# Optimization experiments

Measured on AMD Instinct MI355X. Metric: run time of the kernel, lower is better.

Reference implementation:

```python
import jax, jax.numpy as jnp
import numpy as np

EMBED_DIM = 1024
N_HEADS = 16
HEAD_DIM = EMBED_DIM // N_HEADS


def setup_inputs() -> dict:
    key = jax.random.key(0)
    k_x, k_wi, k_bi, k_wo, k_bo = jax.random.split(key, 5)
    B, N, C = 4, 2048, EMBED_DIM
    scale = 1.0 / np.sqrt(C)
    return {
        "x": jax.random.normal(k_x, (B, N, C), dtype=jnp.float32),
        "w_in": jax.random.normal(k_wi, (C, 3 * C), dtype=jnp.float32) * scale,
        "b_in": jax.random.normal(k_bi, (3 * C,), dtype=jnp.float32) * 0.01,
        "w_out": jax.random.normal(k_wo, (C, C), dtype=jnp.float32) * scale,
        "b_out": jax.random.normal(k_bo, (C,), dtype=jnp.float32) * 0.01,
    }


def reference(x, w_in, b_in, w_out, b_out):
    B, N, C = x.shape
    H, D = N_HEADS, HEAD_DIM
    qkv = x @ w_in + b_in  # (B, N, 3C)
    q, k, v = jnp.split(qkv, 3, axis=-1)
    # (B, H, N, D)
    q = q.reshape(B, N, H, D).transpose(0, 2, 1, 3)
    k = k.reshape(B, N, H, D).transpose(0, 2, 1, 3)
    v = v.reshape(B, N, H, D).transpose(0, 2, 1, 3)
    # Naive attention: full (B,H,N,N) scores, NO sqrt(d) scaling (as in source)
    scores = jnp.einsum("bhnd,bhmd->bhnm", q, k)
    attn = jax.nn.softmax(scores, axis=-1)
    out = jnp.einsum("bhnm,bhmd->bhnd", attn, v)
    out = out.transpose(0, 2, 1, 3).reshape(B, N, C)
    return out @ w_out + b_out
```

## Files before the change

kernel.cpp:

```cpp
#include <hip/hip_runtime.h>
#include <stdint.h>

typedef __attribute__((ext_vector_type(8))) __bf16 bf8v;
typedef __attribute__((ext_vector_type(4))) float f4v;

__device__ __forceinline__ unsigned short f2bf(float f) {
  union { float f; unsigned u; } v; v.f = f;
  unsigned r = v.u + 0x7fffu + ((v.u >> 16) & 1u);
  return (unsigned short)(r >> 16);
}

__device__ __forceinline__ unsigned pk2bf(float f0, float f1) {
  union { float f; unsigned u; } a, b; a.f = f0; b.f = f1;
  unsigned r0 = a.u + 0x7fffu + ((a.u >> 16) & 1u);
  unsigned r1 = b.u + 0x7fffu + ((b.u >> 16) & 1u);
  return __builtin_amdgcn_perm(r1, r0, 0x07060302u);
}

__device__ __forceinline__ void gl_lds16(const void* g, void* l) {
  __builtin_amdgcn_global_load_lds(
      (__attribute__((address_space(1))) void*)(g),
      (__attribute__((address_space(3))) void*)(l), 16, 0, 0);
}

__global__ void cast_bf16_kernel(const float* __restrict__ in,
                                 unsigned short* __restrict__ out) {
  int i = blockIdx.x * 256 + threadIdx.x;
  float4 v = ((const float4*)in)[i];
  ushort4 o;
  o.x = f2bf(v.x); o.y = f2bf(v.y); o.z = f2bf(v.z); o.w = f2bf(v.w);
  ((ushort4*)out)[i] = o;
}

__global__ void transpose_cast_kernel(const float* __restrict__ in,
                                      unsigned short* __restrict__ out,
                                      int R, int C) {
  __shared__ float tile[32][33];
  int c0 = blockIdx.x * 32, r0 = blockIdx.y * 32;
  int tx = threadIdx.x, ty = threadIdx.y;
#pragma unroll
  for (int j = 0; j < 4; ++j)
    tile[ty + 8 * j][tx] = in[(size_t)(r0 + ty + 8 * j) * C + c0 + tx];
  __syncthreads();
#pragma unroll
  for (int j = 0; j < 4; ++j)
    out[(size_t)(c0 + ty + 8 * j) * R + r0 + tx] = f2bf(tile[tx][ty + 8 * j]);
}

__global__ void transpose_v_kernel(const unsigned short* __restrict__ qkv,
                                   unsigned short* __restrict__ vtg) {
  __shared__ unsigned short tile[32][33];
  int bh = blockIdx.z;
  int d0 = blockIdx.y * 32;
  int n0 = blockIdx.x * 32;
  int b = bh >> 4, h = bh & 15;
  int tx = threadIdx.x, ty = threadIdx.y;
  const unsigned short* src = qkv + (size_t)b * 2048 * 3072 + 2048 + h * 64 + d0;
#pragma unroll
  for (int j = 0; j < 4; ++j)
    tile[ty + 8 * j][tx] = src[(size_t)(n0 + ty + 8 * j) * 3072 + tx];
  __syncthreads();
  unsigned short* dst = vtg + ((size_t)bh * 64) * 2048;
#pragma unroll
  for (int j = 0; j < 4; ++j)
    dst[(size_t)(d0 + ty + 8 * j) * 2048 + n0 + tx] = tile[tx][ty + 8 * j];
}

template <bool OUT_BF16>
__global__ __launch_bounds__(256, 2) void gemm_bt(
    const unsigned short* __restrict__ A,
    const unsigned short* __restrict__ BT,
    const float* __restrict__ bias,
    void* __restrict__ Cp,
    int M, int N, int K) {
  __shared__ __align__(16) unsigned short As[128 * 32];
  __shared__ __align__(16) unsigned short Bs[128 * 32];
  const int tid = threadIdx.x;
  const int wave = tid >> 6, lane = tid & 63;
  const int lo = lane & 15, hi = lane >> 4;
  const int m0 = blockIdx.y * 128, n0 = blockIdx.x * 128;
  const int wm = (wave >> 1) * 64, wn = (wave & 1) * 64;

  f4v acc[4][4] = {};

  const int srow = lane >> 2;
  const int scol = (lane & 3) * 8;

  for (int k0 = 0; k0 < K; k0 += 32) {
#pragma unroll
    for (int p = 0; p < 2; ++p) {
      int r = p * 64 + wave * 16 + srow;
      gl_lds16(A + (size_t)(m0 + r) * K + k0 + scol,
               &As[(p * 64 + wave * 16) * 32]);
      gl_lds16(BT + (size_t)(n0 + r) * K + k0 + scol,
               &Bs[(p * 64 + wave * 16) * 32]);
    }
    __syncthreads();
    bf8v a[4], b[4];
#pragma unroll
    for (int i = 0; i < 4; ++i)
      a[i] = *(const bf8v*)&As[(wm + i * 16 + lo) * 32 + hi * 8];
#pragma unroll
    for (int j = 0; j < 4; ++j)
      b[j] = *(const bf8v*)&Bs[(wn + j * 16 + lo) * 32 + hi * 8];
#pragma unroll
    for (int i = 0; i < 4; ++i)
#pragma unroll
      for (int j = 0; j < 4; ++j)
        acc[i][j] = __builtin_amdgcn_mfma_f32_16x16x32_bf16(a[i], b[j], acc[i][j], 0, 0, 0);
    __syncthreads();
  }

#pragma unroll
  for (int i = 0; i < 4; ++i) {
#pragma unroll
    for (int r = 0; r < 4; ++r) {
      int row = m0 + wm + i * 16 + hi * 4 + r;
#pragma unroll
      for (int j = 0; j < 4; ++j) {
        int col = n0 + wn + j * 16 + lo;
        float v = acc[i][j][r] + bias[col];
        if (OUT_BF16)
          ((unsigned short*)Cp)[(size_t)row * N + col] = f2bf(v);
        else
          ((float*)Cp)[(size_t)row * N + col] = v;
      }
    }
  }
}

#define FSTR 72

__global__ __launch_bounds__(256, 4) void flash_attn(
    const unsigned short* __restrict__ qkv,
    const unsigned short* __restrict__ vtg,
    unsigned short* __restrict__ y) {
  __shared__ __align__(16) unsigned short Ps[128 * FSTR];
  __shared__ __align__(16) unsigned short Kt[64 * FSTR];
  __shared__ __align__(16) unsigned short Vt[64 * FSTR];
  const int tid = threadIdx.x;
  const int wave = tid >> 6, lane = tid & 63;
  const int lo = lane & 15, hi = lane >> 4;
  const int b = blockIdx.z, h = blockIdx.y, q0 = blockIdx.x * 128;
  const size_t base = (size_t)b * 2048 * 3072;
  const int qoff = h * 64, koff = 1024 + h * 64;
  const unsigned short* vsrc = vtg + (size_t)(b * 16 + h) * 64 * 2048;

#pragma unroll
  for (int i = 0; i < 4; ++i) {
    int cid = i * 256 + tid;
    int m = cid >> 3, c = cid & 7;
    *(float4*)&Ps[m * FSTR + c * 8] =
        *(const float4*)(qkv + base + (size_t)(q0 + m) * 3072 + qoff + c * 8);
  }
  __syncthreads();
  bf8v bq[2][2];
#pragma unroll
  for (int qt = 0; qt < 2; ++qt)
#pragma unroll
    for (int ks = 0; ks < 2; ++ks)
      bq[qt][ks] = *(const bf8v*)&Ps[(wave * 32 + qt * 16 + lo) * FSTR + ks * 32 + hi * 8];
  __syncthreads();

  f4v O[2][4] = {};
  float l_st[2] = {0.f, 0.f};

  for (int kt = 0; kt < 32; ++kt) {
    const int mb = kt * 64;
#pragma unroll
    for (int i = 0; i < 2; ++i) {
      int cid = i * 256 + tid;
      int m = cid >> 3, c = cid & 7;
      *(float4*)&Kt[m * FSTR + c * 8] =
          *(const float4*)(qkv + base + (size_t)(mb + m) * 3072 + koff + c * 8);
      *(float4*)&Vt[m * FSTR + c * 8] =
          *(const float4*)(vsrc + (size_t)m * 2048 + mb + c * 8);
    }
    __syncthreads();

    f4v s2[4][2] = {};
#pragma unroll
    for (int ks = 0; ks < 2; ++ks) {
#pragma unroll
      for (int ct = 0; ct < 4; ++ct) {
        bf8v ak = *(const bf8v*)&Kt[(ct * 16 + lo) * FSTR + ks * 32 + hi * 8];
        s2[ct][0] = __builtin_amdgcn_mfma_f32_16x16x32_bf16(ak, bq[0][ks], s2[ct][0], 0, 0, 0);
        s2[ct][1] = __builtin_amdgcn_mfma_f32_16x16x32_bf16(ak, bq[1][ks], s2[ct][1], 0, 0, 0);
      }
    }

#pragma unroll
    for (int qt = 0; qt < 2; ++qt) {
      int prow = (wave * 32 + qt * 16 + lo) * FSTR;
#pragma unroll
      for (int ct = 0; ct < 4; ++ct) {
        float p0 = __expf(s2[ct][qt][0]);
        float p1 = __expf(s2[ct][qt][1]);
        float p2 = __expf(s2[ct][qt][2]);
        float p3 = __expf(s2[ct][qt][3]);
        l_st[qt] += (p0 + p1) + (p2 + p3);
        uint2 w;
        w.x = pk2bf(p0, p1);
        w.y = pk2bf(p2, p3);
        *(uint2*)&Ps[prow + ct * 16 + hi * 4] = w;
      }
    }

#pragma unroll
    for (int ks = 0; ks < 2; ++ks) {
      bf8v ap0 = *(const bf8v*)&Ps[(wave * 32 + lo) * FSTR + ks * 32 + hi * 8];
      bf8v ap1 = *(const bf8v*)&Ps[(wave * 32 + 16 + lo) * FSTR + ks * 32 + hi * 8];
#pragma unroll
      for (int dt = 0; dt < 4; ++dt) {
        bf8v bv = *(const bf8v*)&Vt[(dt * 16 + lo) * FSTR + ks * 32 + hi * 8];
        O[0][dt] = __builtin_amdgcn_mfma_f32_16x16x32_bf16(ap0, bv, O[0][dt], 0, 0, 0);
        O[1][dt] = __builtin_amdgcn_mfma_f32_16x16x32_bf16(ap1, bv, O[1][dt], 0, 0, 0);
      }
    }
    __syncthreads();
  }

#pragma unroll
  for (int qt = 0; qt < 2; ++qt) {
    float lt = l_st[qt];
    lt += __shfl_xor(lt, 16);
    lt += __shfl_xor(lt, 32);
    l_st[qt] = lt;
  }
#pragma unroll
  for (int qt = 0; qt < 2; ++qt) {
#pragma unroll
    for (int r = 0; r < 4; ++r) {
      float lr = __shfl(l_st[qt], hi * 4 + r);
      float inv = 1.f / lr;
      int row = q0 + wave * 32 + qt * 16 + hi * 4 + r;
      size_t orow = ((size_t)b * 2048 + row) * 1024 + h * 64;
#pragma unroll
      for (int dt = 0; dt < 4; ++dt)
        y[orow + dt * 16 + lo] = f2bf(O[qt][dt][r] * inv);
    }
  }
}

extern "C" void kernel_launch(void* const* d_in, const int* in_sizes, int n_in,
                              void* d_out, int out_size, void* d_ws, size_t ws_size,
                              hipStream_t stream) {
  (void)in_sizes; (void)n_in; (void)out_size; (void)ws_size;
  const float* x     = (const float*)d_in[0];
  const float* w_in  = (const float*)d_in[1];
  const float* b_in  = (const float*)d_in[2];
  const float* w_out = (const float*)d_in[3];
  const float* b_out = (const float*)d_in[4];

  unsigned short* xb  = (unsigned short*)d_ws;
  unsigned short* wiT = xb  + (size_t)8192 * 1024;
  unsigned short* woT = wiT + (size_t)3072 * 1024;
  unsigned short* qkv = woT + (size_t)1024 * 1024;
  unsigned short* yb  = qkv + (size_t)8192 * 3072;
  unsigned short* vtg = xb;

  cast_bf16_kernel<<<8192, 256, 0, stream>>>(x, xb);
  transpose_cast_kernel<<<dim3(96, 32), dim3(32, 8), 0, stream>>>(w_in, wiT, 1024, 3072);
  transpose_cast_kernel<<<dim3(32, 32), dim3(32, 8), 0, stream>>>(w_out, woT, 1024, 1024);

  gemm_bt<true><<<dim3(24, 64), 256, 0, stream>>>(xb, wiT, b_in, qkv, 8192, 3072, 1024);
  transpose_v_kernel<<<dim3(64, 2, 64), dim3(32, 8), 0, stream>>>(qkv, vtg);
  flash_attn<<<dim3(16, 16, 4), 256, 0, stream>>>(qkv, vtg, yb);
  gemm_bt<false><<<dim3(8, 64), 256, 0, stream>>>(yb, woT, b_out, d_out, 8192, 1024, 1024);
}
```

Before: 316.7 us.

## Fold log2e into Q projection, use hw exp2, merge weight transposes, smaller out-proj tiles

Pre-scales the Q columns of the QKV projection by log2(e) so the attention softmax can use the hardware exp2 instruction instead of __expf. Merges the two weight transpose-cast launches into one kernel. Adds a 64x128-tile output-projection GEMM to double the block count for the smaller N=1024 GEMM, and switches bf16 packing to the HIP intrinsic. Rounding Q after scaling slightly changes numerics.

```diff
diff --git a/kernel.cpp b/kernel.cpp
--- a/kernel.cpp
+++ b/kernel.cpp
@@ -1,8 +1,11 @@
 #include <hip/hip_runtime.h>
+#include <hip/hip_bf16.h>
 #include <stdint.h>
 
 typedef __attribute__((ext_vector_type(8))) __bf16 bf8v;
 typedef __attribute__((ext_vector_type(4))) float f4v;
+
+#define L2E 1.44269504088896f
 
 __device__ __forceinline__ unsigned short f2bf(float f) {
   union { float f; unsigned u; } v; v.f = f;
@@ -11,10 +14,13 @@
 }
 
 __device__ __forceinline__ unsigned pk2bf(float f0, float f1) {
-  union { float f; unsigned u; } a, b; a.f = f0; b.f = f1;
-  unsigned r0 = a.u + 0x7fffu + ((a.u >> 16) & 1u);
-  unsigned r1 = b.u + 0x7fffu + ((b.u >> 16) & 1u);
-  return __builtin_amdgcn_perm(r1, r0, 0x07060302u);
+  union { __hip_bfloat162 h; unsigned u; } c;
+  c.h = __float22bfloat162_rn(make_float2(f0, f1));
+  return c.u;
+}
+
+__device__ __forceinline__ float exp2_hw(float x) {
+  return __builtin_amdgcn_exp2f(x);
 }
 
 __device__ __forceinline__ void gl_lds16(const void* g, void* l) {
@@ -32,11 +38,16 @@
   ((ushort4*)out)[i] = o;
 }
 
-__global__ void transpose_cast_kernel(const float* __restrict__ in,
-                                      unsigned short* __restrict__ out,
-                                      int R, int C) {
+__global__ void transpose_w_kernel(const float* __restrict__ w_in,
+                                   const float* __restrict__ w_out,
+                                   unsigned short* __restrict__ wiT,
+                                   unsigned short* __restrict__ woT) {
   __shared__ float tile[32][33];
-  int c0 = blockIdx.x * 32, r0 = blockIdx.y * 32;
+  int bx = blockIdx.x;
+  const float* in; unsigned short* out; int C, c0;
+  if (bx < 96) { in = w_in;  out = wiT; C = 3072; c0 = bx * 32; }
+  else         { in = w_out; out = woT; C = 1024; c0 = (bx - 96) * 32; }
+  int r0 = blockIdx.y * 32;
   int tx = threadIdx.x, ty = threadIdx.y;
 #pragma unroll
   for (int j = 0; j < 4; ++j)
@@ -44,7 +55,7 @@
   __syncthreads();
 #pragma unroll
   for (int j = 0; j < 4; ++j)
-    out[(size_t)(c0 + ty + 8 * j) * R + r0 + tx] = f2bf(tile[tx][ty + 8 * j]);
+    out[(size_t)(c0 + ty + 8 * j) * 1024 + r0 + tx] = f2bf(tile[tx][ty + 8 * j]);
 }
 
 __global__ void transpose_v_kernel(const unsigned short* __restrict__ qkv,
@@ -66,13 +77,12 @@
     dst[(size_t)(d0 + ty + 8 * j) * 2048 + n0 + tx] = tile[tx][ty + 8 * j];
 }
 
-template <bool OUT_BF16>
 __global__ __launch_bounds__(256, 2) void gemm_bt(
     const unsigned short* __restrict__ A,
     const unsigned short* __restrict__ BT,
     const float* __restrict__ bias,
-    void* __restrict__ Cp,
-    int M, int N, int K) {
+    unsigned short* __restrict__ C,
+    int M, int N, int K, int scale_ncols, float scale) {
   __shared__ __align__(16) unsigned short As[128 * 32];
   __shared__ __align__(16) unsigned short Bs[128 * 32];
   const int tid = threadIdx.x;
@@ -120,10 +130,66 @@
       for (int j = 0; j < 4; ++j) {
         int col = n0 + wn + j * 16 + lo;
         float v = acc[i][j][r] + bias[col];
-        if (OUT_BF16)
-          ((unsigned short*)Cp)[(size_t)row * N + col] = f2bf(v);
-        else
-          ((float*)Cp)[(size_t)row * N + col] = v;
+        if (col < scale_ncols) v *= scale;
+        C[(size_t)row * N + col] = f2bf(v);
+      }
+    }
+  }
+}
+
+__global__ __launch_bounds__(256, 4) void gemm_bt_sm(
+    const unsigned short* __restrict__ A,
+    const unsigned short* __restrict__ BT,
+    const float* __restrict__ bias,
+    float* __restrict__ C,
+    int M, int N, int K) {
+  __shared__ __align__(16) unsigned short As[64 * 32];
+  __shared__ __align__(16) unsigned short Bs[128 * 32];
+  const int tid = threadIdx.x;
+  const int wave = tid >> 6, lane = tid & 63;
+  const int lo = lane & 15, hi = lane >> 4;
+  const int m0 = blockIdx.y * 64, n0 = blockIdx.x * 128;
+  const int wm = (wave >> 1) * 32, wn = (wave & 1) * 64;
+
+  f4v acc[2][4] = {};
+
+  const int srow = lane >> 2;
+  const int scol = (lane & 3) * 8;
+
+  for (int k0 = 0; k0 < K; k0 += 32) {
+    gl_lds16(A + (size_t)(m0 + wave * 16 + srow) * K + k0 + scol,
+             &As[(wave * 16) * 32]);
+#pragma unroll
+    for (int p = 0; p < 2; ++p) {
+      int r = p * 64 + wave * 16 + srow;
+      gl_lds16(BT + (size_t)(n0 + r) * K + k0 + scol,
+               &Bs[(p * 64 + wave * 16) * 32]);
+    }
+    __syncthreads();
+    bf8v a[2], b[4];
+#pragma unroll
+    for (int i = 0; i < 2; ++i)
+      a[i] = *(const bf8v*)&As[(wm + i * 16 + lo) * 32 + hi * 8];
+#pragma unroll
+    for (int j = 0; j < 4; ++j)
+      b[j] = *(const bf8v*)&Bs[(wn + j * 16 + lo) * 32 + hi * 8];
+#pragma unroll
+    for (int i = 0; i < 2; ++i)
+#pragma unroll
+      for (int j = 0; j < 4; ++j)
+        acc[i][j] = __builtin_amdgcn_mfma_f32_16x16x32_bf16(a[i], b[j], acc[i][j], 0, 0, 0);
+    __syncthreads();
+  }
+
+#pragma unroll
+  for (int i = 0; i < 2; ++i) {
+#pragma unroll
+    for (int r = 0; r < 4; ++r) {
+      int row = m0 + wm + i * 16 + hi * 4 + r;
+#pragma unroll
+      for (int j = 0; j < 4; ++j) {
+        int col = n0 + wn + j * 16 + lo;
+        C[(size_t)row * N + col] = acc[i][j][r] + bias[col];
       }
     }
   }
@@ -194,10 +260,10 @@
       int prow = (wave * 32 + qt * 16 + lo) * FSTR;
 #pragma unroll
       for (int ct = 0; ct < 4; ++ct) {
-        float p0 = __expf(s2[ct][qt][0]);
-        float p1 = __expf(s2[ct][qt][1]);
-        float p2 = __expf(s2[ct][qt][2]);
-        float p3 = __expf(s2[ct][qt][3]);
+        float p0 = exp2_hw(s2[ct][qt][0]);
+        float p1 = exp2_hw(s2[ct][qt][1]);
+        float p2 = exp2_hw(s2[ct][qt][2]);
+        float p3 = exp2_hw(s2[ct][qt][3]);
         l_st[qt] += (p0 + p1) + (p2 + p3);
         uint2 w;
         w.x = pk2bf(p0, p1);
@@ -260,11 +326,12 @@
   unsigned short* vtg = xb;
 
   cast_bf16_kernel<<<8192, 256, 0, stream>>>(x, xb);
-  transpose_cast_kernel<<<dim3(96, 32), dim3(32, 8), 0, stream>>>(w_in, wiT, 1024, 3072);
-  transpose_cast_kernel<<<dim3(32, 32), dim3(32, 8), 0, stream>>>(w_out, woT, 1024, 1024);
-
-  gemm_bt<true><<<dim3(24, 64), 256, 0, stream>>>(xb, wiT, b_in, qkv, 8192, 3072, 1024);
+  transpose_w_kernel<<<dim3(128, 32), dim3(32, 8), 0, stream>>>(w_in, w_out, wiT, woT);
+
+  gemm_bt<<<dim3(24, 64), 256, 0, stream>>>(xb, wiT, b_in, qkv, 8192, 3072, 1024,
+                                            1024, L2E);
   transpose_v_kernel<<<dim3(64, 2, 64), dim3(32, 8), 0, stream>>>(qkv, vtg);
   flash_attn<<<dim3(16, 16, 4), 256, 0, stream>>>(qkv, vtg, yb);
-  gemm_bt<false><<<dim3(8, 64), 256, 0, stream>>>(yb, woT, b_out, d_out, 8192, 1024, 1024);
-}
+  gemm_bt_sm<<<dim3(8, 128), 256, 0, stream>>>(yb, woT, b_out, (float*)d_out,
+                                               8192, 1024, 1024);
+}
```

Result: faster. 304.2 us (-3.9%).
